# Optimization experiments

Measured on AMD Instinct MI355X. Metric: run time of the kernel, lower is better.

Reference implementation:

```python
import jax, jax.numpy as jnp
import numpy as np

V, C, L, NH, NKV, HID, E, K, T, B = 32000, 1536, 2, 12, 4, 2048, 8, 2, 2048, 1
D = C // NH  # 128
NREP = NH // NKV
EPS = 1e-6

def _rms(x, w):
    return x * jax.lax.rsqrt(jnp.mean(x * x, axis=-1, keepdims=True) + EPS) * w


def setup_inputs() -> dict:
    key = jax.random.key(0)
    ks = jax.random.split(key, 14)
    s = 0.02
    inp = {
        "tokens": jax.random.randint(ks[0], (B, T), 0, V, dtype=jnp.int64),
        "emb": jax.random.normal(ks[1], (V, C), jnp.float32) * s,      # tied with output proj
        "pos": jax.random.normal(ks[2], (T, C), jnp.float32) * s,
        "wq": jax.random.normal(ks[3], (L, C, NH * D), jnp.float32) * s,
        "wk": jax.random.normal(ks[4], (L, C, NKV * D), jnp.float32) * s,
        "wv": jax.random.normal(ks[5], (L, C, NKV * D), jnp.float32) * s,
        "wo": jax.random.normal(ks[6], (L, C, C), jnp.float32) * s,
        "attn_norm_w": jnp.ones((L, C), jnp.float32),
        "ffn_norm_w": jnp.ones((L, C), jnp.float32),
        "gate": jax.random.normal(ks[7], (L, C, E), jnp.float32) * s,
        "ew1": jax.random.normal(ks[8], (L, E, C, HID), jnp.float32) * s,
        "ew2": jax.random.normal(ks[9], (L, E, HID, C), jnp.float32) * s,
        "ew3": jax.random.normal(ks[10], (L, E, C, HID), jnp.float32) * s,
        "final_norm_w": jnp.ones((C,), jnp.float32),
    }
    return inp


def _forward(tokens, emb, pos, wq, wk, wv, wo, attn_norm_w, ffn_norm_w, gate,
             ew1, ew2, ew3, final_norm_w):
    x = emb[tokens] + pos[None, :T]            # [B,T,C]; dropout=0 (eval)
    causal = jnp.tril(jnp.ones((T, T), bool))
    for l in range(L):
        # --- GQA attention ---
        h = _rms(x, attn_norm_w[l])
        q = (h @ wq[l]).reshape(B, T, NH, D).transpose(0, 2, 1, 3)     # [B,NH,T,D]
        k = (h @ wk[l]).reshape(B, T, NKV, D).transpose(0, 2, 1, 3)
        v = (h @ wv[l]).reshape(B, T, NKV, D).transpose(0, 2, 1, 3)
        k = jnp.repeat(k, NREP, axis=1)
        v = jnp.repeat(v, NREP, axis=1)
        scores = jnp.einsum("bhqd,bhkd->bhqk", q, k) / jnp.sqrt(jnp.float32(D))
        scores = jnp.where(causal, scores, jnp.finfo(scores.dtype).min)
        attn = jax.nn.softmax(scores, axis=-1)
        y = jnp.einsum("bhqk,bhkd->bhqd", attn, v)
        y = y.transpose(0, 2, 1, 3).reshape(B, T, C)
        x = x + y @ wo[l]
        # --- MoE FFN (top-k routed SwiGLU experts) ---
        xf = _rms(x, ffn_norm_w[l]).reshape(-1, C)                      # [N,C]
        probs = jax.nn.softmax(xf @ gate[l], axis=-1)                   # [N,E]
        topw, topi = jax.lax.top_k(probs, K)
        topw = topw / jnp.sum(topw, axis=-1, keepdims=True)
        dense_w = jnp.sum(jax.nn.one_hot(topi, E, dtype=xf.dtype) * topw[..., None], axis=1)  # [N,E]
        h1 = jnp.einsum("nc,ech->enh", xf, ew1[l])
        h3 = jnp.einsum("nc,ech->enh", xf, ew3[l])
        hh = jax.nn.silu(h1) * h3                                       # [E,N,HID]
        moe = jnp.einsum("ne,enh,ehc->nc", dense_w, hh, ew2[l])
        x = x + moe.reshape(B, T, C)
    x = _rms(x, final_norm_w)
    logits = x @ emb.T                                                   # tied output proj
    return logits


def reference(tokens, emb, pos, wq, wk, wv, wo, attn_norm_w, ffn_norm_w, gate,
              ew1, ew2, ew3, final_norm_w):
    return _forward(tokens, emb, pos, wq, wk, wv, wo, attn_norm_w, ffn_norm_w,
                    gate, ew1, ew2, ew3, final_norm_w)
```

## Files before the change

kernel.cpp:

```cpp
#include <hip/hip_runtime.h>
#include <hip/hip_bf16.h>
#include <math.h>

#define Tn   2048
#define Cn   1536
#define Vn   32000
#define NHn  12
#define NKVn 4
#define Dn   128
#define HIDn 2048
#define En   8
#define Kn   2
#define Ln   2
#define NREPn 3
#define EPSn 1e-6f
#define CHT  16
#define NCHn 4

using bf16 = __hip_bfloat16;
using bf16x8 = __attribute__((ext_vector_type(8))) short;
using f32x4v = __attribute__((ext_vector_type(4))) float;

__device__ __forceinline__ void split3(float v, short& h, short& m, short& lo) {
  bf16 b0 = __float2bfloat16(v);
  float r1 = v - __bfloat162float(b0);
  bf16 b1 = __float2bfloat16(r1);
  float r2 = r1 - __bfloat162float(b1);
  bf16 b2 = __float2bfloat16(r2);
  h = *reinterpret_cast<short*>(&b0);
  m = *reinterpret_cast<short*>(&b1);
  lo = *reinterpret_cast<short*>(&b2);
}
__device__ __forceinline__ float b2f(short s) {
  bf16 b = *reinterpret_cast<bf16*>(&s);
  return __bfloat162float(b);
}
__device__ __forceinline__ void gl_lds16(const void* g, void* l) {
  __builtin_amdgcn_global_load_lds((const __attribute__((address_space(1))) void*)g,
                                   (__attribute__((address_space(3))) void*)l, 16, 0, 0);
}

__global__ void embed_k(const int* __restrict__ tok, const float* __restrict__ emb,
                        const float* __restrict__ pos, float* __restrict__ x) {
  int n = blockIdx.x;
  int t = threadIdx.x;
  int id = tok[n];
  const float* er = emb + (size_t)id * Cn;
  const float* pr = pos + (size_t)n * Cn;
  float* xr = x + (size_t)n * Cn;
  for (int c = t; c < Cn; c += 256) xr[c] = er[c] + pr[c];
}

__global__ void rmsnorm_k(const float* __restrict__ x, const float* __restrict__ w,
                          float* __restrict__ out) {
  int n = blockIdx.x, t = threadIdx.x;
  const float* xr = x + (size_t)n * Cn;
  float v[6];
  float ss = 0.f;
#pragma unroll
  for (int i = 0; i < 6; i++) { v[i] = xr[t + i * 256]; ss += v[i] * v[i]; }
  for (int off = 32; off > 0; off >>= 1) ss += __shfl_down(ss, off, 64);
  __shared__ float red[4];
  __shared__ float rtot;
  int wave = t >> 6, lane = t & 63;
  if (lane == 0) red[wave] = ss;
  __syncthreads();
  if (t == 0) rtot = rsqrtf((red[0] + red[1] + red[2] + red[3]) / (float)Cn + EPSn);
  __syncthreads();
  float r = rtot;
  float* orow = out + (size_t)n * Cn;
#pragma unroll
  for (int i = 0; i < 6; i++) { int c = t + i * 256; orow[c] = v[i] * r * w[c]; }
}

__global__ void f2b_k(const float* __restrict__ s, bf16* __restrict__ d, size_t n4) {
  size_t i = (size_t)blockIdx.x * 256 + threadIdx.x;
  size_t stride = (size_t)gridDim.x * 256;
  for (; i < n4; i += stride) {
    float4 v = ((const float4*)s)[i];
    d[i * 4 + 0] = __float2bfloat16(v.x);
    d[i * 4 + 1] = __float2bfloat16(v.y);
    d[i * 4 + 2] = __float2bfloat16(v.z);
    d[i * 4 + 3] = __float2bfloat16(v.w);
  }
}

__global__ void splita_k(const float* __restrict__ s, short* __restrict__ dh,
                         short* __restrict__ dm, short* __restrict__ dl, size_t n4) {
  size_t i = (size_t)blockIdx.x * 256 + threadIdx.x;
  size_t stride = (size_t)gridDim.x * 256;
  for (; i < n4; i += stride) {
    float4 v = ((const float4*)s)[i];
    float a[4] = {v.x, v.y, v.z, v.w};
#pragma unroll
    for (int u = 0; u < 4; u++) {
      short h, m, lo;
      split3(a[u], h, m, lo);
      dh[i * 4 + u] = h; dm[i * 4 + u] = m; dl[i * 4 + u] = lo;
    }
  }
}

__global__ void transp3_k(const float* __restrict__ src, short* __restrict__ dh,
                          short* __restrict__ dm, short* __restrict__ dl, int K, int N) {
  __shared__ __align__(16) float ls[32][33];
// ... 133 lines not shown
      int ro = (wc + j * 16 + rl) * 32 + ko;
      bf16x8 bh = *(const bf16x8*)(sBH + ro);
      bf16x8 bm_ = *(const bf16x8*)(sBM + ro);
      bf16x8 bl = *(const bf16x8*)(sBL + ro);
#pragma unroll
      for (int i = 0; i < 4; i++) {
        acc[i][j] = __builtin_amdgcn_mfma_f32_16x16x32_bf16(aL[i], bh, acc[i][j], 0, 0, 0);
        acc[i][j] = __builtin_amdgcn_mfma_f32_16x16x32_bf16(aH[i], bl, acc[i][j], 0, 0, 0);
        acc[i][j] = __builtin_amdgcn_mfma_f32_16x16x32_bf16(aM[i], bm_, acc[i][j], 0, 0, 0);
        acc[i][j] = __builtin_amdgcn_mfma_f32_16x16x32_bf16(aM[i], bh, acc[i][j], 0, 0, 0);
        acc[i][j] = __builtin_amdgcn_mfma_f32_16x16x32_bf16(aH[i], bm_, acc[i][j], 0, 0, 0);
        acc[i][j] = __builtin_amdgcn_mfma_f32_16x16x32_bf16(aH[i], bh, acc[i][j], 0, 0, 0);
      }
    }
    __syncthreads();
  }
#pragma unroll
  for (int i = 0; i < 4; i++) {
    int rbase = bm + wr + i * 16 + (l >> 4) * 4;
#pragma unroll
    for (int j = 0; j < 4; j++) {
      int col = bn + wc + j * 16 + (l & 15);
#pragma unroll
      for (int r = 0; r < 4; r++) {
        size_t idx = (size_t)(rbase + r) * N + col;
        float v = acc[i][j][r];
        if (res) v += res[idx];
        Co[idx] = v;
      }
    }
  }
}

__global__ void __launch_bounds__(256) mexp6(const bf16* __restrict__ AH, const bf16* __restrict__ AM,
                                             const bf16* __restrict__ AL,
                                             const bf16* __restrict__ BH, const bf16* __restrict__ BM,
                                             const bf16* __restrict__ BL,
                                             const int* __restrict__ perm, const int* __restrict__ cnt,
                                             int ebase,
                                             short* __restrict__ HH, short* __restrict__ HM,
                                             short* __restrict__ HL,
                                             float* __restrict__ Co, int K, int N, int mode) {
  int e = ebase + blockIdx.z;
  int nrows = cnt[e];
  int bm = blockIdx.x * 128;
  if (bm >= nrows) return;
  int bn = blockIdx.y * 128;
  size_t eoff = (size_t)blockIdx.z * K * N;
  __shared__ __align__(16) bf16 sAH[128 * 32], sAM[128 * 32], sAL[128 * 32];
  __shared__ __align__(16) bf16 sBH[128 * 32], sBM[128 * 32], sBL[128 * 32];
  __shared__ int prow[128];
  int t = threadIdx.x, l = t & 63, w = t >> 6;
  if (t < 128) {
    int i = bm + t;
    prow[t] = (i < nrows) ? perm[e * Tn + i] : -1;
  }
  __syncthreads();
  int wr = (w >> 1) * 64, wc = (w & 1) * 64;
  const f32x4v zero = {0.f, 0.f, 0.f, 0.f};
  f32x4v acc[4][4];
#pragma unroll
  for (int i = 0; i < 4; i++)
#pragma unroll
    for (int j = 0; j < 4; j++) acc[i][j] = zero;
  int p0 = prow[t >> 2], p1 = prow[64 + (t >> 2)];
  int g0r = (p0 >= 0) ? (mode == 2 ? p0 : (p0 >> 1)) : 0;
  int g1r = (p1 >= 0) ? (mode == 2 ? p1 : (p1 >> 1)) : 0;
  size_t a0 = (size_t)g0r * K + (t & 3) * 8;
  size_t a1 = (size_t)g1r * K + (t & 3) * 8;
  size_t b0 = eoff + (size_t)(bn + (t >> 2)) * K + (t & 3) * 8;
  size_t b1 = eoff + (size_t)(bn + 64 + (t >> 2)) * K + (t & 3) * 8;
  int rl = l & 15, ko = (l >> 4) * 8;
  for (int k0 = 0; k0 < K; k0 += 32) {
    gl_lds16(AH + a0 + k0, (char*)sAH + t * 16);
    gl_lds16(AH + a1 + k0, (char*)sAH + (256 + t) * 16);
    gl_lds16(AM + a0 + k0, (char*)sAM + t * 16);
    gl_lds16(AM + a1 + k0, (char*)sAM + (256 + t) * 16);
    gl_lds16(AL + a0 + k0, (char*)sAL + t * 16);
    gl_lds16(AL + a1 + k0, (char*)sAL + (256 + t) * 16);
    gl_lds16(BH + b0 + k0, (char*)sBH + t * 16);
    gl_lds16(BH + b1 + k0, (char*)sBH + (256 + t) * 16);
    gl_lds16(BM + b0 + k0, (char*)sBM + t * 16);
    gl_lds16(BM + b1 + k0, (char*)sBM + (256 + t) * 16);
    gl_lds16(BL + b0 + k0, (char*)sBL + t * 16);
    gl_lds16(BL + b1 + k0, (char*)sBL + (256 + t) * 16);
    __syncthreads();
    bf16x8 aH[4], aM[4], aL[4];
#pragma unroll
    for (int i = 0; i < 4; i++) {
      int ro = (wr + i * 16 + rl) * 32 + ko;
      aH[i] = *(const bf16x8*)(sAH + ro);
      aM[i] = *(const bf16x8*)(sAM + ro);
      aL[i] = *(const bf16x8*)(sAL + ro);
    }
#pragma unroll
    for (int j = 0; j < 4; j++) {
      int ro = (wc + j * 16 + rl) * 32 + ko;
      bf16x8 bh = *(const bf16x8*)(sBH + ro);
      bf16x8 bm_ = *(const bf16x8*)(sBM + ro);
      bf16x8 bl = *(const bf16x8*)(sBL + ro);
#pragma unroll
      for (int i = 0; i < 4; i++) {
        acc[i][j] = __builtin_amdgcn_mfma_f32_16x16x32_bf16(aL[i], bh, acc[i][j], 0, 0, 0);
        acc[i][j] = __builtin_amdgcn_mfma_f32_16x16x32_bf16(aH[i], bl, acc[i][j], 0, 0, 0);
        acc[i][j] = __builtin_amdgcn_mfma_f32_16x16x32_bf16(aM[i], bm_, acc[i][j], 0, 0, 0);
        acc[i][j] = __builtin_amdgcn_mfma_f32_16x16x32_bf16(aM[i], bh, acc[i][j], 0, 0, 0);
        acc[i][j] = __builtin_amdgcn_mfma_f32_16x16x32_bf16(aH[i], bm_, acc[i][j], 0, 0, 0);
        acc[i][j] = __builtin_amdgcn_mfma_f32_16x16x32_bf16(aH[i], bh, acc[i][j], 0, 0, 0);
      }
    }
    __syncthreads();
  }
#pragma unroll
  for (int i = 0; i < 4; i++) {
#pragma unroll
    for (int r = 0; r < 4; r++) {
      int lrow = wr + i * 16 + (l >> 4) * 4 + r;
      int p = prow[lrow];
      if (p < 0) continue;
#pragma unroll
      for (int j = 0; j < 4; j++) {
        int col = bn + wc + j * 16 + (l & 15);
        size_t idx = (size_t)p * N + col;
        float v = acc[i][j][r];
        if (mode == 0) {
          short h, m, lo;
          split3(v, h, m, lo);
          HH[idx] = h; HM[idx] = m; HL[idx] = lo;
        } else if (mode == 1) {
          float v1 = b2f(HH[idx]) + b2f(HM[idx]) + b2f(HL[idx]);
          float hh = (v1 / (1.f + expf(-v1))) * v;
          short h, m, lo;
          split3(hh, h, m, lo);
          HH[idx] = h; HM[idx] = m; HL[idx] = lo;
        } else {
          Co[idx] = v;
        }
      }
    }
  }
}

__global__ void __launch_bounds__(256) mexpB(const bf16* __restrict__ A, const bf16* __restrict__ B,
                                             const int* __restrict__ perm, const int* __restrict__ cnt,
                                             int ebase, bf16* __restrict__ HB,
                                             float* __restrict__ Co, int K, int N, int mode) {
  int e = ebase + blockIdx.z;
  int nrows = cnt[e];
  int bm = blockIdx.x * 128;
  if (bm >= nrows) return;
  int bn = blockIdx.y * 128;
  size_t eoff = (size_t)blockIdx.z * K * N;
  __shared__ __align__(16) bf16 sA[128 * 32];
  __shared__ __align__(16) bf16 sB[128 * 32];
  __shared__ int prow[128];
  int t = threadIdx.x, l = t & 63, w = t >> 6;
  if (t < 128) {
    int i = bm + t;
    prow[t] = (i < nrows) ? perm[e * Tn + i] : -1;
  }
  __syncthreads();
  int wr = (w >> 1) * 64, wc = (w & 1) * 64;
  const f32x4v zero = {0.f, 0.f, 0.f, 0.f};
  f32x4v acc[4][4];
#pragma unroll
  for (int i = 0; i < 4; i++)
#pragma unroll
    for (int j = 0; j < 4; j++) acc[i][j] = zero;
  int p0 = prow[t >> 2], p1 = prow[64 + (t >> 2)];
  int g0r = (p0 >= 0) ? (mode == 2 ? p0 : (p0 >> 1)) : 0;
  int g1r = (p1 >= 0) ? (mode == 2 ? p1 : (p1 >> 1)) : 0;
  size_t a0 = (size_t)g0r * K + (t & 3) * 8;
  size_t a1 = (size_t)g1r * K + (t & 3) * 8;
  size_t b0 = eoff + (size_t)(bn + (t >> 2)) * K + (t & 3) * 8;
  size_t b1 = eoff + (size_t)(bn + 64 + (t >> 2)) * K + (t & 3) * 8;
  int rl = l & 15, ko = (l >> 4) * 8;
  for (int k0 = 0; k0 < K; k0 += 32) {
    gl_lds16(A + a0 + k0, (char*)sA + t * 16);
    gl_lds16(A + a1 + k0, (char*)sA + (256 + t) * 16);
    gl_lds16(B + b0 + k0, (char*)sB + t * 16);
    gl_lds16(B + b1 + k0, (char*)sB + (256 + t) * 16);
    __syncthreads();
    bf16x8 a[4], b[4];
#pragma unroll
    for (int i = 0; i < 4; i++) a[i] = *(const bf16x8*)(sA + (wr + i * 16 + rl) * 32 + ko);
#pragma unroll
    for (int j = 0; j < 4; j++) b[j] = *(const bf16x8*)(sB + (wc + j * 16 + rl) * 32 + ko);
#pragma unroll
    for (int i = 0; i < 4; i++)
#pragma unroll
      for (int j = 0; j < 4; j++)
        acc[i][j] = __builtin_amdgcn_mfma_f32_16x16x32_bf16(a[i], b[j], acc[i][j], 0, 0, 0);
    __syncthreads();
  }
#pragma unroll
  for (int i = 0; i < 4; i++) {
#pragma unroll
    for (int r = 0; r < 4; r++) {
      int lrow = wr + i * 16 + (l >> 4) * 4 + r;
      int p = prow[lrow];
      if (p < 0) continue;
#pragma unroll
      for (int j = 0; j < 4; j++) {
        int col = bn + wc + j * 16 + (l & 15);
        size_t idx = (size_t)p * N + col;
        float v = acc[i][j][r];
        if (mode == 0) {
          HB[idx] = __float2bfloat16(v);
        } else if (mode == 1) {
          float v1 = __bfloat162float(HB[idx]);
          HB[idx] = __float2bfloat16((v1 / (1.f + expf(-v1))) * v);
        } else {
          Co[idx] = v;
        }
      }
    }
  }
}

__global__ void __launch_bounds__(256) attn_part_k(const float* __restrict__ q,
                                                   const float* __restrict__ k,
                                                   const float* __restrict__ v,
                                                   float* __restrict__ po,
                                                   float* __restrict__ pm,
                                                   float* __restrict__ pl) {
  int qt = blockIdx.x;
  int head = blockIdx.y;
  int ch = blockIdx.z;
  int ntiles = qt + 1;
  int tA = ch * CHT;
  if (tA >= ntiles) return;
  int tB = tA + CHT < ntiles ? tA + CHT : ntiles;
  int kvh = head / NREPn;
  int q0 = qt * 32;
  int t = threadIdx.x;
  int r = t >> 3, g = t & 7, d0 = g * 16;
  int row = q0 + r;
  __shared__ __align__(16) float ks[32][Dn + 4];
  __shared__ __align__(16) float vs[32][Dn + 4];
  const float scale = 0.08838834764831845f;
  float qr[16];
  {
    const float* qrow = q + (size_t)row * (NHn * Dn) + head * Dn + d0;
#pragma unroll
    for (int j = 0; j < 16; j += 4) {
      float4 u = *(const float4*)(qrow + j);
      qr[j] = u.x * scale; qr[j + 1] = u.y * scale;
      qr[j + 2] = u.z * scale; qr[j + 3] = u.w * scale;
    }
  }
  float o[16];
#pragma unroll
  for (int j = 0; j < 16; j++) o[j] = 0.f;
  float rowm = -1e30f, rowl = 0.f;

  for (int kt = tA; kt < tB; kt++) {
    int kv0 = kt * 32;
    for (int e = t; e < 32 * 32; e += 256) {
      int rr = e >> 5, c4 = (e & 31) * 4;
      size_t off = (size_t)(kv0 + rr) * (NKVn * Dn) + kvh * Dn + c4;
      *(float4*)&ks[rr][c4] = *(const float4*)(k + off);
      *(float4*)&vs[rr][c4] = *(const float4*)(v + off);
    }
    __syncthreads();
    float s[32];
#pragma unroll
    for (int kk = 0; kk < 32; kk++) {
      const float* krow = &ks[kk][d0];
      float p = 0.f;
#pragma unroll
      for (int j = 0; j < 16; j += 4) {
        float4 u = *(const float4*)(krow + j);
        p += qr[j] * u.x + qr[j + 1] * u.y + qr[j + 2] * u.z + qr[j + 3] * u.w;
      }
      p += __shfl_xor(p, 1);
      p += __shfl_xor(p, 2);
      p += __shfl_xor(p, 4);
      s[kk] = p;
    }
    if (kt == qt) {
#pragma unroll
      for (int kk = 0; kk < 32; kk++)
        if (kk > r) s[kk] = -1e30f;
    }
    float mx = s[0];
#pragma unroll
    for (int kk = 1; kk < 32; kk++) mx = fmaxf(mx, s[kk]);
    float m_new = fmaxf(rowm, mx);
    float corr = expf(rowm - m_new);
    float sum = 0.f;
#pragma unroll
    for (int kk = 0; kk < 32; kk++) { s[kk] = expf(s[kk] - m_new); sum += s[kk]; }
    rowl = rowl * corr + sum;
    rowm = m_new;
#pragma unroll
// ... 128 lines not shown
  const float* pos    = (const float*)d_in[2];
  const float* wq     = (const float*)d_in[3];
  const float* wk     = (const float*)d_in[4];
  const float* wv     = (const float*)d_in[5];
  const float* wo     = (const float*)d_in[6];
  const float* attn_nw= (const float*)d_in[7];
  const float* ffn_nw = (const float*)d_in[8];
  const float* gate   = (const float*)d_in[9];
  const float* ew1    = (const float*)d_in[10];
  const float* ew2    = (const float*)d_in[11];
  const float* ew3    = (const float*)d_in[12];
  const float* final_nw = (const float*)d_in[13];
  float* out = (float*)d_out;

  char* wsb = (char*)d_ws;
  const size_t NC = (size_t)Tn * Cn;
  size_t off = 0;
  auto alloc = [&](size_t bytes) -> size_t {
    off = (off + 255) & ~(size_t)255;
    size_t p = off;
    off += bytes;
    return p;
  };
  size_t o_x    = alloc(NC * 4);
  size_t o_h    = alloc(NC * 4);
  size_t o_gl   = alloc((size_t)Tn * En * 4);
  size_t o_topw = alloc((size_t)Tn * Kn * 4);
  size_t o_cnt  = alloc(64);
  size_t o_perm = alloc((size_t)En * Tn * 4);
  size_t wlvl   = (size_t)4 * Cn * HIDn * 2;
  size_t o_w    = alloc(3 * wlvl);
  size_t hs_lvl = NC * 2;
  size_t o_hs   = alloc(3 * hs_lvl);
  size_t o_qb   = alloc(NC * 4);
  size_t o_kb   = alloc((size_t)Tn * NKVn * Dn * 4);
  size_t o_vb   = alloc((size_t)Tn * NKVn * Dn * 4);
  size_t o_yb   = alloc(NC * 4);
  size_t hb_lvl = (size_t)Tn * Kn * HIDn * 2;
  size_t o_hbs  = o_qb;
  size_t end_hbs = o_hbs + 3 * hb_lvl;
  if (off < end_hbs) off = end_hbs;
  size_t o_pair = alloc(NC * 4);
  size_t o_po   = alloc((size_t)NHn * Tn * NCHn * Dn * 4);
  size_t o_pm   = alloc((size_t)NHn * Tn * NCHn * 4);
  size_t o_pl   = alloc((size_t)NHn * Tn * NCHn * 4);

  float* x       = (float*)(wsb + o_x);
  float* h       = (float*)(wsb + o_h);
  float* gl      = (float*)(wsb + o_gl);
  float* topw    = (float*)(wsb + o_topw);
  int*   cnt     = (int*)(wsb + o_cnt);
  int*   perm    = (int*)(wsb + o_perm);
  float* qb      = (float*)(wsb + o_qb);
  float* kb      = (float*)(wsb + o_kb);
  float* vb      = (float*)(wsb + o_vb);
  float* yb      = (float*)(wsb + o_yb);
  float* pairout = (float*)(wsb + o_pair);
  bf16*  hb      = (bf16*)(wsb + o_pair);
  bf16*  embB    = (bf16*)(wsb + o_w);
  float* po      = (float*)(wsb + o_po);
  float* pm      = (float*)(wsb + o_pm);
  float* pl      = (float*)(wsb + o_pl);

  short* hs[3]; short* hbs[3]; short* ewT[3];
  for (int s = 0; s < 3; s++) {
    hs[s]  = (short*)(wsb + o_hs + (size_t)s * hs_lvl);
    hbs[s] = (short*)(wsb + o_hbs + (size_t)s * hb_lvl);
    ewT[s] = (short*)(wsb + o_w + (size_t)s * wlvl);
  }
  size_t wq_lvl = (size_t)Cn * (NHn * Dn) * 2;
  size_t wk_lvl = (size_t)Cn * (NKVn * Dn) * 2;
  short* wqT[3]; short* wkT[3]; short* wvT[3]; short* woT[3];
  {
    size_t p = o_w;
    for (int s = 0; s < 3; s++) { wqT[s] = (short*)(wsb + p); p += wq_lvl; }
    for (int s = 0; s < 3; s++) { wkT[s] = (short*)(wsb + p); p += wk_lvl; }
    for (int s = 0; s < 3; s++) { wvT[s] = (short*)(wsb + p); p += wk_lvl; }
    for (int s = 0; s < 3; s++) { woT[s] = (short*)(wsb + p); p += wq_lvl; }
  }

  embed_k<<<Tn, 256, 0, stream>>>(tokens, emb, pos, x);
  for (int l = 0; l < Ln; l++) {
    const float* wq_l = wq + (size_t)l * Cn * (NHn * Dn);
    const float* wk_l = wk + (size_t)l * Cn * (NKVn * Dn);
    const float* wv_l = wv + (size_t)l * Cn * (NKVn * Dn);
    const float* wo_l = wo + (size_t)l * Cn * Cn;
    const float* g_l  = gate + (size_t)l * Cn * En;
    const float* e1_l = ew1 + (size_t)l * En * Cn * HIDn;
    const float* e2_l = ew2 + (size_t)l * En * HIDn * Cn;
    const float* e3_l = ew3 + (size_t)l * En * Cn * HIDn;

    transp3_k<<<dim3(Cn / 32, (NHn * Dn) / 32, 1), 256, 0, stream>>>(wq_l, wqT[0], wqT[1], wqT[2], Cn, NHn * Dn);
    transp3_k<<<dim3(Cn / 32, (NKVn * Dn) / 32, 1), 256, 0, stream>>>(wk_l, wkT[0], wkT[1], wkT[2], Cn, NKVn * Dn);
    transp3_k<<<dim3(Cn / 32, (NKVn * Dn) / 32, 1), 256, 0, stream>>>(wv_l, wvT[0], wvT[1], wvT[2], Cn, NKVn * Dn);
    transp3_k<<<dim3(Cn / 32, Cn / 32, 1), 256, 0, stream>>>(wo_l, woT[0], woT[1], woT[2], Cn, Cn);
    rmsnorm_k<<<Tn, 256, 0, stream>>>(x, attn_nw + (size_t)l * Cn, h);
    splita_k<<<2048, 256, 0, stream>>>(h, hs[0], hs[1], hs[2], NC / 4);
    gemm6<<<dim3(Tn / 128, (NHn * Dn) / 128), 256, 0, stream>>>(
        (bf16*)hs[0], (bf16*)hs[1], (bf16*)hs[2], (bf16*)wqT[0], (bf16*)wqT[1], (bf16*)wqT[2],
        nullptr, qb, Tn, NHn * Dn, Cn);
    gemm6<<<dim3(Tn / 128, (NKVn * Dn) / 128), 256, 0, stream>>>(
        (bf16*)hs[0], (bf16*)hs[1], (bf16*)hs[2], (bf16*)wkT[0], (bf16*)wkT[1], (bf16*)wkT[2],
        nullptr, kb, Tn, NKVn * Dn, Cn);
    gemm6<<<dim3(Tn / 128, (NKVn * Dn) / 128), 256, 0, stream>>>(
        (bf16*)hs[0], (bf16*)hs[1], (bf16*)hs[2], (bf16*)wvT[0], (bf16*)wvT[1], (bf16*)wvT[2],
        nullptr, vb, Tn, NKVn * Dn, Cn);
    attn_part_k<<<dim3(Tn / 32, NHn, NCHn), 256, 0, stream>>>(qb, kb, vb, po, pm, pl);
    attn_merge_k<<<dim3(Tn / 32, NHn), 256, 0, stream>>>(po, pm, pl, yb);
    splita_k<<<2048, 256, 0, stream>>>(yb, hs[0], hs[1], hs[2], NC / 4);
    gemm6<<<dim3(Tn / 128, Cn / 128), 256, 0, stream>>>(
        (bf16*)hs[0], (bf16*)hs[1], (bf16*)hs[2], (bf16*)woT[0], (bf16*)woT[1], (bf16*)woT[2],
        x, x, Tn, Cn, Cn);

    rmsnorm_k<<<Tn, 256, 0, stream>>>(x, ffn_nw + (size_t)l * Cn, h);
    gate_k<<<Tn, 256, 0, stream>>>(h, g_l, gl);
    hipMemsetAsync(cnt, 0, 64, stream);
    route_k<<<Tn / 256, 256, 0, stream>>>(gl, topw, cnt, perm);

    if (l < Ln - 1) {
      splita_k<<<2048, 256, 0, stream>>>(h, hs[0], hs[1], hs[2], NC / 4);
      for (int half = 0; half < 2; half++) {
        size_t hoff = (size_t)half * 4 * Cn * HIDn;
        int eb = half * 4;
        transp3_k<<<dim3(Cn / 32, HIDn / 32, 4), 256, 0, stream>>>(e1_l + hoff, ewT[0], ewT[1], ewT[2], Cn, HIDn);
        mexp6<<<dim3(Tn / 128, HIDn / 128, 4), 256, 0, stream>>>(
            (bf16*)hs[0], (bf16*)hs[1], (bf16*)hs[2], (bf16*)ewT[0], (bf16*)ewT[1], (bf16*)ewT[2],
            perm, cnt, eb, hbs[0], hbs[1], hbs[2], nullptr, Cn, HIDn, 0);
        transp3_k<<<dim3(Cn / 32, HIDn / 32, 4), 256, 0, stream>>>(e3_l + hoff, ewT[0], ewT[1], ewT[2], Cn, HIDn);
        mexp6<<<dim3(Tn / 128, HIDn / 128, 4), 256, 0, stream>>>(
            (bf16*)hs[0], (bf16*)hs[1], (bf16*)hs[2], (bf16*)ewT[0], (bf16*)ewT[1], (bf16*)ewT[2],
            perm, cnt, eb, hbs[0], hbs[1], hbs[2], nullptr, Cn, HIDn, 1);
        transp3_k<<<dim3(HIDn / 32, Cn / 32, 4), 256, 0, stream>>>(e2_l + hoff, ewT[0], ewT[1], ewT[2], HIDn, Cn);
        mexp6<<<dim3(Tn / 128, Cn / 128, 4), 256, 0, stream>>>(
            (bf16*)hbs[0], (bf16*)hbs[1], (bf16*)hbs[2], (bf16*)ewT[0], (bf16*)ewT[1], (bf16*)ewT[2],
            perm, cnt, eb, hbs[0], hbs[1], hbs[2], pairout, HIDn, Cn, 2);
      }
    } else {
      f2b_k<<<2048, 256, 0, stream>>>(h, (bf16*)hs[0], NC / 4);
      for (int half = 0; half < 2; half++) {
        size_t hoff = (size_t)half * 4 * Cn * HIDn;
        int eb = half * 4;
        transp_k<<<dim3(Cn / 32, HIDn / 32, 4), 256, 0, stream>>>(e1_l + hoff, (bf16*)ewT[0], Cn, HIDn);
        mexpB<<<dim3(Tn / 128, HIDn / 128, 4), 256, 0, stream>>>(
            (bf16*)hs[0], (bf16*)ewT[0], perm, cnt, eb, (bf16*)hbs[0], nullptr, Cn, HIDn, 0);
        transp_k<<<dim3(Cn / 32, HIDn / 32, 4), 256, 0, stream>>>(e3_l + hoff, (bf16*)ewT[0], Cn, HIDn);
        mexpB<<<dim3(Tn / 128, HIDn / 128, 4), 256, 0, stream>>>(
            (bf16*)hs[0], (bf16*)ewT[0], perm, cnt, eb, (bf16*)hbs[0], nullptr, Cn, HIDn, 1);
        transp_k<<<dim3(HIDn / 32, Cn / 32, 4), 256, 0, stream>>>(e2_l + hoff, (bf16*)ewT[0], HIDn, Cn);
        mexpB<<<dim3(Tn / 128, Cn / 128, 4), 256, 0, stream>>>(
            (bf16*)hbs[0], (bf16*)ewT[0], perm, cnt, eb, (bf16*)hbs[0], pairout, HIDn, Cn, 2);
      }
    }
    combine_k<<<Tn, 256, 0, stream>>>(pairout, topw, x);
  }
  rmsnorm_k<<<Tn, 256, 0, stream>>>(x, final_nw, h);
  f2b_k<<<2048, 256, 0, stream>>>(h, hb, NC / 4);
  f2b_k<<<2048, 256, 0, stream>>>(emb, embB, (size_t)Vn * Cn / 4);
  gemm_btl<<<dim3(Tn / 128, Vn / 128), 256, 0, stream>>>(hb, embB, nullptr, out, Tn, Vn, Cn);
}
```

Baseline: 5.301 ms.

## Fuse QKV projections, dual gate/up expert GEMMs, and rmsnorm with split conversion

Concatenates the Q, K and V weights into one transposed matrix so a single GEMM writes a packed QKV buffer, which attention reads at fixed offsets. The expert w1 and w3 GEMMs are merged into one kernel that keeps two accumulators and applies SiLU-multiply in its epilogue, so the activation is no longer written, read back and re-split. RMSNorm now emits the bf16 or three-way bf16 split directly, removing separate splita and f2b passes. The cost is higher register and LDS use in the dual kernels, which may lower occupancy, and the split-precision expert path is now processed two experts at a time.

```diff
diff --git a/kernel.cpp b/kernel.cpp
--- a/kernel.cpp
+++ b/kernel.cpp
@@ -16,6 +16,7 @@
 #define EPSn 1e-6f
 #define CHT  16
 #define NCHn 4
+#define QKVW 2560
 
 using bf16 = __hip_bfloat16;
 using bf16x8 = __attribute__((ext_vector_type(8))) short;
@@ -51,8 +52,9 @@
   for (int c = t; c < Cn; c += 256) xr[c] = er[c] + pr[c];
 }
 
-__global__ void rmsnorm_k(const float* __restrict__ x, const float* __restrict__ w,
-                          float* __restrict__ out) {
+__global__ void rms3_k(const float* __restrict__ x, const float* __restrict__ w,
+                       float* __restrict__ outf, short* __restrict__ dh,
+                       short* __restrict__ dm, short* __restrict__ dl) {
   int n = blockIdx.x, t = threadIdx.x;
   const float* xr = x + (size_t)n * Cn;
   float v[6];
@@ -68,9 +70,43 @@
   if (t == 0) rtot = rsqrtf((red[0] + red[1] + red[2] + red[3]) / (float)Cn + EPSn);
   __syncthreads();
   float r = rtot;
-  float* orow = out + (size_t)n * Cn;
-#pragma unroll
-  for (int i = 0; i < 6; i++) { int c = t + i * 256; orow[c] = v[i] * r * w[c]; }
+#pragma unroll
+  for (int i = 0; i < 6; i++) {
+    int c = t + i * 256;
+    float val = v[i] * r * w[c];
+    size_t idx = (size_t)n * Cn + c;
+    if (outf) outf[idx] = val;
+    short h, m, lo;
+    split3(val, h, m, lo);
+    dh[idx] = h; dm[idx] = m; dl[idx] = lo;
+  }
+}
+
+__global__ void rmsb_k(const float* __restrict__ x, const float* __restrict__ w,
+                       float* __restrict__ outf, bf16* __restrict__ outb) {
+  int n = blockIdx.x, t = threadIdx.x;
+  const float* xr = x + (size_t)n * Cn;
+  float v[6];
+  float ss = 0.f;
+#pragma unroll
+  for (int i = 0; i < 6; i++) { v[i] = xr[t + i * 256]; ss += v[i] * v[i]; }
+  for (int off = 32; off > 0; off >>= 1) ss += __shfl_down(ss, off, 64);
+  __shared__ float red[4];
+  __shared__ float rtot;
+  int wave = t >> 6, lane = t & 63;
+  if (lane == 0) red[wave] = ss;
+  __syncthreads();
+  if (t == 0) rtot = rsqrtf((red[0] + red[1] + red[2] + red[3]) / (float)Cn + EPSn);
+  __syncthreads();
+  float r = rtot;
+#pragma unroll
+  for (int i = 0; i < 6; i++) {
+    int c = t + i * 256;
+    float val = v[i] * r * w[c];
+    size_t idx = (size_t)n * Cn + c;
+    if (outf) outf[idx] = val;
+    outb[idx] = __float2bfloat16(val);
+  }
 }
 
 __global__ void f2b_k(const float* __restrict__ s, bf16* __restrict__ d, size_t n4) {
@@ -270,15 +306,132 @@
   }
 }
 
+__global__ void __launch_bounds__(256) mexp6d(const bf16* __restrict__ AH, const bf16* __restrict__ AM,
+                                              const bf16* __restrict__ AL,
+                                              const bf16* __restrict__ B1H, const bf16* __restrict__ B1M,
+                                              const bf16* __restrict__ B1L,
+                                              const bf16* __restrict__ B3H, const bf16* __restrict__ B3M,
+                                              const bf16* __restrict__ B3L,
+                                              const int* __restrict__ perm, const int* __restrict__ cnt,
+                                              int ebase,
+                                              short* __restrict__ HH, short* __restrict__ HM,
+                                              short* __restrict__ HL, int K, int N) {
+  int e = ebase + blockIdx.z;
+  int nrows = cnt[e];
+  int bm = blockIdx.x * 128;
+  if (bm >= nrows) return;
+  int bn = blockIdx.y * 128;
+  size_t eoff = (size_t)blockIdx.z * K * N;
+  __shared__ __align__(16) bf16 sAH[128 * 32], sAM[128 * 32], sAL[128 * 32];
+  __shared__ __align__(16) bf16 s1H[128 * 32], s1M[128 * 32], s1L[128 * 32];
+  __shared__ __align__(16) bf16 s3H[128 * 32], s3M[128 * 32], s3L[128 * 32];
+  __shared__ int prow[128];
+  int t = threadIdx.x, l = t & 63, w = t >> 6;
+  if (t < 128) {
+    int i = bm + t;
+    prow[t] = (i < nrows) ? perm[e * Tn + i] : -1;
+  }
+  __syncthreads();
+  int wr = (w >> 1) * 64, wc = (w & 1) * 64;
+  const f32x4v zero = {0.f, 0.f, 0.f, 0.f};
+  f32x4v acc1[4][4], acc3[4][4];
+#pragma unroll
+  for (int i = 0; i < 4; i++)
+#pragma unroll
+    for (int j = 0; j < 4; j++) { acc1[i][j] = zero; acc3[i][j] = zero; }
+  int p0 = prow[t >> 2], p1 = prow[64 + (t >> 2)];
+  int g0r = (p0 >= 0) ? (p0 >> 1) : 0;
+  int g1r = (p1 >= 0) ? (p1 >> 1) : 0;
+  size_t a0 = (size_t)g0r * K + (t & 3) * 8;
+  size_t a1 = (size_t)g1r * K + (t & 3) * 8;
+  size_t b0 = eoff + (size_t)(bn + (t >> 2)) * K + (t & 3) * 8;
+  size_t b1 = eoff + (size_t)(bn + 64 + (t >> 2)) * K + (t & 3) * 8;
+  int rl = l & 15, ko = (l >> 4) * 8;
+  for (int k0 = 0; k0 < K; k0 += 32) {
+    gl_lds16(AH + a0 + k0, (char*)sAH + t * 16);
+    gl_lds16(AH + a1 + k0, (char*)sAH + (256 + t) * 16);
+    gl_lds16(AM + a0 + k0, (char*)sAM + t * 16);
+    gl_lds16(AM + a1 + k0, (char*)sAM + (256 + t) * 16);
+    gl_lds16(AL + a0 + k0, (char*)sAL + t * 16);
+    gl_lds16(AL + a1 + k0, (char*)sAL + (256 + t) * 16);
+    gl_lds16(B1H + b0 + k0, (char*)s1H + t * 16);
+    gl_lds16(B1H + b1 + k0, (char*)s1H + (256 + t) * 16);
+    gl_lds16(B1M + b0 + k0, (char*)s1M + t * 16);
+    gl_lds16(B1M + b1 + k0, (char*)s1M + (256 + t) * 16);
+    gl_lds16(B1L + b0 + k0, (char*)s1L + t * 16);
+    gl_lds16(B1L + b1 + k0, (char*)s1L + (256 + t) * 16);
+    gl_lds16(B3H + b0 + k0, (char*)s3H + t * 16);
+    gl_lds16(B3H + b1 + k0, (char*)s3H + (256 + t) * 16);
+    gl_lds16(B3M + b0 + k0, (char*)s3M + t * 16);
+    gl_lds16(B3M + b1 + k0, (char*)s3M + (256 + t) * 16);
+    gl_lds16(B3L + b0 + k0, (char*)s3L + t * 16);
+    gl_lds16(B3L + b1 + k0, (char*)s3L + (256 + t) * 16);
+    __syncthreads();
+    bf16x8 aH[4], aM[4], aL[4];
+#pragma unroll
+    for (int i = 0; i < 4; i++) {
+      int ro = (wr + i * 16 + rl) * 32 + ko;
+      aH[i] = *(const bf16x8*)(sAH + ro);
+      aM[i] = *(const bf16x8*)(sAM + ro);
+      aL[i] = *(const bf16x8*)(sAL + ro);
+    }
+#pragma unroll
+    for (int j = 0; j < 4; j++) {
+      int ro = (wc + j * 16 + rl) * 32 + ko;
+      bf16x8 bh = *(const bf16x8*)(s1H + ro);
+      bf16x8 bm_ = *(const bf16x8*)(s1M + ro);
+      bf16x8 bl = *(const bf16x8*)(s1L + ro);
+#pragma unroll
+      for (int i = 0; i < 4; i++) {
+        acc1[i][j] = __builtin_amdgcn_mfma_f32_16x16x32_bf16(aL[i], bh, acc1[i][j], 0, 0, 0);
+        acc1[i][j] = __builtin_amdgcn_mfma_f32_16x16x32_bf16(aH[i], bl, acc1[i][j], 0, 0, 0);
+        acc1[i][j] = __builtin_amdgcn_mfma_f32_16x16x32_bf16(aM[i], bm_, acc1[i][j], 0, 0, 0);
+        acc1[i][j] = __builtin_amdgcn_mfma_f32_16x16x32_bf16(aM[i], bh, acc1[i][j], 0, 0, 0);
+        acc1[i][j] = __builtin_amdgcn_mfma_f32_16x16x32_bf16(aH[i], bm_, acc1[i][j], 0, 0, 0);
+        acc1[i][j] = __builtin_amdgcn_mfma_f32_16x16x32_bf16(aH[i], bh, acc1[i][j], 0, 0, 0);
+      }
+      bh = *(const bf16x8*)(s3H + ro);
+      bm_ = *(const bf16x8*)(s3M + ro);
+      bl = *(const bf16x8*)(s3L + ro);
+#pragma unroll
+      for (int i = 0; i < 4; i++) {
+        acc3[i][j] = __builtin_amdgcn_mfma_f32_16x16x32_bf16(aL[i], bh, acc3[i][j], 0, 0, 0);
+        acc3[i][j] = __builtin_amdgcn_mfma_f32_16x16x32_bf16(aH[i], bl, acc3[i][j], 0, 0, 0);
+        acc3[i][j] = __builtin_amdgcn_mfma_f32_16x16x32_bf16(aM[i], bm_, acc3[i][j], 0, 0, 0);
+        acc3[i][j] = __builtin_amdgcn_mfma_f32_16x16x32_bf16(aM[i], bh, acc3[i][j], 0, 0, 0);
+        acc3[i][j] = __builtin_amdgcn_mfma_f32_16x16x32_bf16(aH[i], bm_, acc3[i][j], 0, 0, 0);
+        acc3[i][j] = __builtin_amdgcn_mfma_f32_16x16x32_bf16(aH[i], bh, acc3[i][j], 0, 0, 0);
+      }
+    }
+    __syncthreads();
+  }
+#pragma unroll
+  for (int i = 0; i < 4; i++) {
+#pragma unroll
+    for (int r = 0; r < 4; r++) {
+      int lrow = wr + i * 16 + (l >> 4) * 4 + r;
+      int p = prow[lrow];
+      if (p < 0) continue;
+#pragma unroll
+      for (int j = 0; j < 4; j++) {
+        int col = bn + wc + j * 16 + (l & 15);
+        size_t idx = (size_t)p * N + col;
+        float h1 = acc1[i][j][r], h3 = acc3[i][j][r];
+        float hh = (h1 / (1.f + expf(-h1))) * h3;
+        short h, m, lo;
+        split3(hh, h, m, lo);
+        HH[idx] = h; HM[idx] = m; HL[idx] = lo;
+      }
+    }
+  }
+}
+
 __global__ void __launch_bounds__(256) mexp6(const bf16* __restrict__ AH, const bf16* __restrict__ AM,
                                              const bf16* __restrict__ AL,
                                              const bf16* __restrict__ BH, const bf16* __restrict__ BM,
                                              const bf16* __restrict__ BL,
                                              const int* __restrict__ perm, const int* __restrict__ cnt,
-                                             int ebase,
-                                             short* __restrict__ HH, short* __restrict__ HM,
-                                             short* __restrict__ HL,
-                                             float* __restrict__ Co, int K, int N, int mode) {
+                                             int ebase, float* __restrict__ Co, int K, int N) {
   int e = ebase + blockIdx.z;
   int nrows = cnt[e];
   int bm = blockIdx.x * 128;
@@ -302,8 +455,8 @@
 #pragma unroll
     for (int j = 0; j < 4; j++) acc[i][j] = zero;
   int p0 = prow[t >> 2], p1 = prow[64 + (t >> 2)];
-  int g0r = (p0 >= 0) ? (mode == 2 ? p0 : (p0 >> 1)) : 0;
-  int g1r = (p1 >= 0) ? (mode == 2 ? p1 : (p1 >> 1)) : 0;
+  int g0r = (p0 >= 0) ? p0 : 0;
+  int g1r = (p1 >= 0) ? p1 : 0;
   size_t a0 = (size_t)g0r * K + (t & 3) * 8;
   size_t a1 = (size_t)g1r * K + (t & 3) * 8;
   size_t b0 = eoff + (size_t)(bn + (t >> 2)) * K + (t & 3) * 8;
@@ -359,21 +512,83 @@
 #pragma unroll
       for (int j = 0; j < 4; j++) {
         int col = bn + wc + j * 16 + (l & 15);
-        size_t idx = (size_t)p * N + col;
-        float v = acc[i][j][r];
-        if (mode == 0) {
-          short h, m, lo;
-          split3(v, h, m, lo);
-          HH[idx] = h; HM[idx] = m; HL[idx] = lo;
-        } else if (mode == 1) {
-          float v1 = b2f(HH[idx]) + b2f(HM[idx]) + b2f(HL[idx]);
-          float hh = (v1 / (1.f + expf(-v1))) * v;
-          short h, m, lo;
-          split3(hh, h, m, lo);
-          HH[idx] = h; HM[idx] = m; HL[idx] = lo;
-        } else {
-          Co[idx] = v;
-        }
+        Co[(size_t)p * N + col] = acc[i][j][r];
+      }
+    }
+  }
+}
+
+__global__ void __launch_bounds__(256) mexpBd(const bf16* __restrict__ A, const bf16* __restrict__ B1,
+                                              const bf16* __restrict__ B3,
+                                              const int* __restrict__ perm, const int* __restrict__ cnt,
+                                              int ebase, bf16* __restrict__ HB, int K, int N) {
+  int e = ebase + blockIdx.z;
+  int nrows = cnt[e];
+  int bm = blockIdx.x * 128;
+  if (bm >= nrows) return;
+  int bn = blockIdx.y * 128;
+  size_t eoff = (size_t)blockIdx.z * K * N;
+  __shared__ __align__(16) bf16 sA[128 * 32];
+  __shared__ __align__(16) bf16 s1[128 * 32];
+  __shared__ __align__(16) bf16 s3[128 * 32];
+  __shared__ int prow[128];
+  int t = threadIdx.x, l = t & 63, w = t >> 6;
+  if (t < 128) {
+    int i = bm + t;
+    prow[t] = (i < nrows) ? perm[e * Tn + i] : -1;
+  }
+  __syncthreads();
+  int wr = (w >> 1) * 64, wc = (w & 1) * 64;
+  const f32x4v zero = {0.f, 0.f, 0.f, 0.f};
+  f32x4v acc1[4][4], acc3[4][4];
+#pragma unroll
+  for (int i = 0; i < 4; i++)
+#pragma unroll
+    for (int j = 0; j < 4; j++) { acc1[i][j] = zero; acc3[i][j] = zero; }
+  int p0 = prow[t >> 2], p1 = prow[64 + (t >> 2)];
+  int g0r = (p0 >= 0) ? (p0 >> 1) : 0;
+  int g1r = (p1 >= 0) ? (p1 >> 1) : 0;
+  size_t a0 = (size_t)g0r * K + (t & 3) * 8;
+  size_t a1 = (size_t)g1r * K + (t & 3) * 8;
+  size_t b0 = eoff + (size_t)(bn + (t >> 2)) * K + (t & 3) * 8;
+  size_t b1 = eoff + (size_t)(bn + 64 + (t >> 2)) * K + (t & 3) * 8;
+  int rl = l & 15, ko = (l >> 4) * 8;
+  for (int k0 = 0; k0 < K; k0 += 32) {
+    gl_lds16(A + a0 + k0, (char*)sA + t * 16);
+    gl_lds16(A + a1 + k0, (char*)sA + (256 + t) * 16);
+    gl_lds16(B1 + b0 + k0, (char*)s1 + t * 16);
+    gl_lds16(B1 + b1 + k0, (char*)s1 + (256 + t) * 16);
+    gl_lds16(B3 + b0 + k0, (char*)s3 + t * 16);
+    gl_lds16(B3 + b1 + k0, (char*)s3 + (256 + t) * 16);
+    __syncthreads();
+    bf16x8 a[4];
+#pragma unroll
+    for (int i = 0; i < 4; i++) a[i] = *(const bf16x8*)(sA + (wr + i * 16 + rl) * 32 + ko);
+#pragma unroll
+    for (int j = 0; j < 4; j++) {
+      int ro = (wc + j * 16 + rl) * 32 + ko;
+      bf16x8 b1v = *(const bf16x8*)(s1 + ro);
+      bf16x8 b3v = *(const bf16x8*)(s3 + ro);
+#pragma unroll
+      for (int i = 0; i < 4; i++) {
+        acc1[i][j] = __builtin_amdgcn_mfma_f32_16x16x32_bf16(a[i], b1v, acc1[i][j], 0, 0, 0);
+        acc3[i][j] = __builtin_amdgcn_mfma_f32_16x16x32_bf16(a[i], b3v, acc3[i][j], 0, 0, 0);
+      }
+    }
+    __syncthreads();
+  }
+#pragma unroll
+  for (int i = 0; i < 4; i++) {
+#pragma unroll
+    for (int r = 0; r < 4; r++) {
+      int lrow = wr + i * 16 + (l >> 4) * 4 + r;
+      int p = prow[lrow];
+      if (p < 0) continue;
+#pragma unroll
+      for (int j = 0; j < 4; j++) {
+        int col = bn + wc + j * 16 + (l & 15);
+        float h1 = acc1[i][j][r], h3 = acc3[i][j][r];
+        HB[(size_t)p * N + col] = __float2bfloat16((h1 / (1.f + expf(-h1))) * h3);
       }
     }
   }
@@ -381,8 +596,7 @@
 
 __global__ void __launch_bounds__(256) mexpB(const bf16* __restrict__ A, const bf16* __restrict__ B,
                                              const int* __restrict__ perm, const int* __restrict__ cnt,
-                                             int ebase, bf16* __restrict__ HB,
-                                             float* __restrict__ Co, int K, int N, int mode) {
+                                             int ebase, float* __restrict__ Co, int K, int N) {
   int e = ebase + blockIdx.z;
   int nrows = cnt[e];
   int bm = blockIdx.x * 128;
@@ -406,8 +620,8 @@
 #pragma unroll
     for (int j = 0; j < 4; j++) acc[i][j] = zero;
   int p0 = prow[t >> 2], p1 = prow[64 + (t >> 2)];
-  int g0r = (p0 >= 0) ? (mode == 2 ? p0 : (p0 >> 1)) : 0;
-  int g1r = (p1 >= 0) ? (mode == 2 ? p1 : (p1 >> 1)) : 0;
+  int g0r = (p0 >= 0) ? p0 : 0;
+  int g1r = (p1 >= 0) ? p1 : 0;
   size_t a0 = (size_t)g0r * K + (t & 3) * 8;
   size_t a1 = (size_t)g1r * K + (t & 3) * 8;
   size_t b0 = eoff + (size_t)(bn + (t >> 2)) * K + (t & 3) * 8;
@@ -441,24 +655,13 @@
 #pragma unroll
       for (int j = 0; j < 4; j++) {
         int col = bn + wc + j * 16 + (l & 15);
-        size_t idx = (size_t)p * N + col;
-        float v = acc[i][j][r];
-        if (mode == 0) {
-          HB[idx] = __float2bfloat16(v);
-        } else if (mode == 1) {
-          float v1 = __bfloat162float(HB[idx]);
-          HB[idx] = __float2bfloat16((v1 / (1.f + expf(-v1))) * v);
-        } else {
-          Co[idx] = v;
-        }
-      }
-    }
-  }
-}
-
-__global__ void __launch_bounds__(256) attn_part_k(const float* __restrict__ q,
-                                                   const float* __restrict__ k,
-                                                   const float* __restrict__ v,
+        Co[(size_t)p * N + col] = acc[i][j][r];
+      }
+    }
+  }
+}
+
+__global__ void __launch_bounds__(256) attn_part_k(const float* __restrict__ qkv,
                                                    float* __restrict__ po,
                                                    float* __restrict__ pm,
                                                    float* __restrict__ pl) {
@@ -479,7 +682,7 @@
   const float scale = 0.08838834764831845f;
   float qr[16];
   {
-    const float* qrow = q + (size_t)row * (NHn * Dn) + head * Dn + d0;
+    const float* qrow = qkv + (size_t)row * QKVW + head * Dn + d0;
 #pragma unroll
     for (int j = 0; j < 16; j += 4) {
       float4 u = *(const float4*)(qrow + j);
@@ -496,9 +699,9 @@
     int kv0 = kt * 32;
     for (int e = t; e < 32 * 32; e += 256) {
       int rr = e >> 5, c4 = (e & 31) * 4;
-      size_t off = (size_t)(kv0 + rr) * (NKVn * Dn) + kvh * Dn + c4;
-      *(float4*)&ks[rr][c4] = *(const float4*)(k + off);
-      *(float4*)&vs[rr][c4] = *(const float4*)(v + off);
+      size_t base = (size_t)(kv0 + rr) * QKVW + kvh * Dn + c4;
+      *(float4*)&ks[rr][c4] = *(const float4*)(qkv + base + 1536);
+      *(float4*)&vs[rr][c4] = *(const float4*)(qkv + base + 2048);
     }
     __syncthreads();
     float s[32];
@@ -693,12 +896,10 @@
   size_t o_w    = alloc(3 * wlvl);
   size_t hs_lvl = NC * 2;
   size_t o_hs   = alloc(3 * hs_lvl);
-  size_t o_qb   = alloc(NC * 4);
-  size_t o_kb   = alloc((size_t)Tn * NKVn * Dn * 4);
-  size_t o_vb   = alloc((size_t)Tn * NKVn * Dn * 4);
+  size_t o_qkv  = alloc((size_t)Tn * QKVW * 4);
   size_t o_yb   = alloc(NC * 4);
   size_t hb_lvl = (size_t)Tn * Kn * HIDn * 2;
-  size_t o_hbs  = o_qb;
+  size_t o_hbs  = o_qkv;
   size_t end_hbs = o_hbs + 3 * hb_lvl;
   if (off < end_hbs) off = end_hbs;
   size_t o_pair = alloc(NC * 4);
@@ -712,9 +913,7 @@
   float* topw    = (float*)(wsb + o_topw);
   int*   cnt     = (int*)(wsb + o_cnt);
   int*   perm    = (int*)(wsb + o_perm);
-  float* qb      = (float*)(wsb + o_qb);
-  float* kb      = (float*)(wsb + o_kb);
-  float* vb      = (float*)(wsb + o_vb);
+  float* qkvb    = (float*)(wsb + o_qkv);
   float* yb      = (float*)(wsb + o_yb);
   float* pairout = (float*)(wsb + o_pair);
   bf16*  hb      = (bf16*)(wsb + o_pair);
@@ -723,22 +922,28 @@
   float* pm      = (float*)(wsb + o_pm);
   float* pl      = (float*)(wsb + o_pl);
 
-  short* hs[3]; short* hbs[3]; short* ewT[3];
+  short* hs[3]; short* hbs[3];
   for (int s = 0; s < 3; s++) {
     hs[s]  = (short*)(wsb + o_hs + (size_t)s * hs_lvl);
     hbs[s] = (short*)(wsb + o_hbs + (size_t)s * hb_lvl);
-    ewT[s] = (short*)(wsb + o_w + (size_t)s * wlvl);
-  }
-  size_t wq_lvl = (size_t)Cn * (NHn * Dn) * 2;
-  size_t wk_lvl = (size_t)Cn * (NKVn * Dn) * 2;
-  short* wqT[3]; short* wkT[3]; short* wvT[3]; short* woT[3];
-  {
-    size_t p = o_w;
-    for (int s = 0; s < 3; s++) { wqT[s] = (short*)(wsb + p); p += wq_lvl; }
-    for (int s = 0; s < 3; s++) { wkT[s] = (short*)(wsb + p); p += wk_lvl; }
-    for (int s = 0; s < 3; s++) { wvT[s] = (short*)(wsb + p); p += wk_lvl; }
-    for (int s = 0; s < 3; s++) { woT[s] = (short*)(wsb + p); p += wq_lvl; }
-  }
+  }
+  size_t qkvw_lvl = (size_t)QKVW * Cn * 2;
+  size_t wo_lvl   = (size_t)Cn * Cn * 2;
+  short* qkvT[3]; short* woT[3];
+  for (int s = 0; s < 3; s++) {
+    qkvT[s] = (short*)(wsb + o_w + (size_t)s * qkvw_lvl);
+    woT[s]  = (short*)(wsb + o_w + 3 * qkvw_lvl + (size_t)s * wo_lvl);
+  }
+  size_t q2lvl = (size_t)2 * Cn * HIDn * 2;
+  short* e1T[3]; short* e3T[3]; short* e2T[3];
+  for (int s = 0; s < 3; s++) {
+    e1T[s] = (short*)(wsb + o_w + (size_t)s * q2lvl);
+    e3T[s] = (short*)(wsb + o_w + 3 * q2lvl + (size_t)s * q2lvl);
+    e2T[s] = (short*)(wsb + o_w + (size_t)s * wlvl);
+  }
+  bf16* ew1B = (bf16*)(wsb + o_w);
+  bf16* ew3B = (bf16*)(wsb + o_w + wlvl);
+  bf16* ew2B = (bf16*)(wsb + o_w);
 
   embed_k<<<Tn, 256, 0, stream>>>(tokens, emb, pos, x);
   for (int l = 0; l < Ln; l++) {
@@ -751,71 +956,67 @@
     const float* e2_l = ew2 + (size_t)l * En * HIDn * Cn;
     const float* e3_l = ew3 + (size_t)l * En * Cn * HIDn;
 
-    transp3_k<<<dim3(Cn / 32, (NHn * Dn) / 32, 1), 256, 0, stream>>>(wq_l, wqT[0], wqT[1], wqT[2], Cn, NHn * Dn);
-    transp3_k<<<dim3(Cn / 32, (NKVn * Dn) / 32, 1), 256, 0, stream>>>(wk_l, wkT[0], wkT[1], wkT[2], Cn, NKVn * Dn);
-    transp3_k<<<dim3(Cn / 32, (NKVn * Dn) / 32, 1), 256, 0, stream>>>(wv_l, wvT[0], wvT[1], wvT[2], Cn, NKVn * Dn);
+    transp3_k<<<dim3(Cn / 32, (NHn * Dn) / 32, 1), 256, 0, stream>>>(wq_l, qkvT[0], qkvT[1], qkvT[2], Cn, NHn * Dn);
+    transp3_k<<<dim3(Cn / 32, (NKVn * Dn) / 32, 1), 256, 0, stream>>>(
+        wk_l, qkvT[0] + (size_t)1536 * Cn, qkvT[1] + (size_t)1536 * Cn, qkvT[2] + (size_t)1536 * Cn, Cn, NKVn * Dn);
+    transp3_k<<<dim3(Cn / 32, (NKVn * Dn) / 32, 1), 256, 0, stream>>>(
+        wv_l, qkvT[0] + (size_t)2048 * Cn, qkvT[1] + (size_t)2048 * Cn, qkvT[2] + (size_t)2048 * Cn, Cn, NKVn * Dn);
     transp3_k<<<dim3(Cn / 32, Cn / 32, 1), 256, 0, stream>>>(wo_l, woT[0], woT[1], woT[2], Cn, Cn);
-    rmsnorm_k<<<Tn, 256, 0, stream>>>(x, attn_nw + (size_t)l * Cn, h);
-    splita_k<<<2048, 256, 0, stream>>>(h, hs[0], hs[1], hs[2], NC / 4);
-    gemm6<<<dim3(Tn / 128, (NHn * Dn) / 128), 256, 0, stream>>>(
-        (bf16*)hs[0], (bf16*)hs[1], (bf16*)hs[2], (bf16*)wqT[0], (bf16*)wqT[1], (bf16*)wqT[2],
-        nullptr, qb, Tn, NHn * Dn, Cn);
-    gemm6<<<dim3(Tn / 128, (NKVn * Dn) / 128), 256, 0, stream>>>(
-        (bf16*)hs[0], (bf16*)hs[1], (bf16*)hs[2], (bf16*)wkT[0], (bf16*)wkT[1], (bf16*)wkT[2],
-        nullptr, kb, Tn, NKVn * Dn, Cn);
-    gemm6<<<dim3(Tn / 128, (NKVn * Dn) / 128), 256, 0, stream>>>(
-        (bf16*)hs[0], (bf16*)hs[1], (bf16*)hs[2], (bf16*)wvT[0], (bf16*)wvT[1], (bf16*)wvT[2],
-        nullptr, vb, Tn, NKVn * Dn, Cn);
-    attn_part_k<<<dim3(Tn / 32, NHn, NCHn), 256, 0, stream>>>(qb, kb, vb, po, pm, pl);
+    rms3_k<<<Tn, 256, 0, stream>>>(x, attn_nw + (size_t)l * Cn, nullptr, hs[0], hs[1], hs[2]);
+    gemm6<<<dim3(Tn / 128, QKVW / 128), 256, 0, stream>>>(
+        (bf16*)hs[0], (bf16*)hs[1], (bf16*)hs[2], (bf16*)qkvT[0], (bf16*)qkvT[1], (bf16*)qkvT[2],
+        nullptr, qkvb, Tn, QKVW, Cn);
+    attn_part_k<<<dim3(Tn / 32, NHn, NCHn), 256, 0, stream>>>(qkvb, po, pm, pl);
     attn_merge_k<<<dim3(Tn / 32, NHn), 256, 0, stream>>>(po, pm, pl, yb);
     splita_k<<<2048, 256, 0, stream>>>(yb, hs[0], hs[1], hs[2], NC / 4);
     gemm6<<<dim3(Tn / 128, Cn / 128), 256, 0, stream>>>(
         (bf16*)hs[0], (bf16*)hs[1], (bf16*)hs[2], (bf16*)woT[0], (bf16*)woT[1], (bf16*)woT[2],
         x, x, Tn, Cn, Cn);
 
-    rmsnorm_k<<<Tn, 256, 0, stream>>>(x, ffn_nw + (size_t)l * Cn, h);
-    gate_k<<<Tn, 256, 0, stream>>>(h, g_l, gl);
-    hipMemsetAsync(cnt, 0, 64, stream);
-    route_k<<<Tn / 256, 256, 0, stream>>>(gl, topw, cnt, perm);
-
     if (l < Ln - 1) {
-      splita_k<<<2048, 256, 0, stream>>>(h, hs[0], hs[1], hs[2], NC / 4);
+      rms3_k<<<Tn, 256, 0, stream>>>(x, ffn_nw + (size_t)l * Cn, h, hs[0], hs[1], hs[2]);
+      gate_k<<<Tn, 256, 0, stream>>>(h, g_l, gl);
+      hipMemsetAsync(cnt, 0, 64, stream);
+      route_k<<<Tn / 256, 256, 0, stream>>>(gl, topw, cnt, perm);
+      for (int q = 0; q < 4; q++) {
+        size_t qoff = (size_t)q * 2 * Cn * HIDn;
+        transp3_k<<<dim3(Cn / 32, HIDn / 32, 2), 256, 0, stream>>>(e1_l + qoff, e1T[0], e1T[1], e1T[2], Cn, HIDn);
+        transp3_k<<<dim3(Cn / 32, HIDn / 32, 2), 256, 0, stream>>>(e3_l + qoff, e3T[0], e3T[1], e3T[2], Cn, HIDn);
+        mexp6d<<<dim3(Tn / 128, HIDn / 128, 2), 256, 0, stream>>>(
+            (bf16*)hs[0], (bf16*)hs[1], (bf16*)hs[2],
+            (bf16*)e1T[0], (bf16*)e1T[1], (bf16*)e1T[2],
+            (bf16*)e3T[0], (bf16*)e3T[1], (bf16*)e3T[2],
+            perm, cnt, q * 2, hbs[0], hbs[1], hbs[2], Cn, HIDn);
+      }
+      for (int half = 0; half < 2; half++) {
+        size_t hoff = (size_t)half * 4 * HIDn * Cn;
+        transp3_k<<<dim3(HIDn / 32, Cn / 32, 4), 256, 0, stream>>>(e2_l + hoff, e2T[0], e2T[1], e2T[2], HIDn, Cn);
+        mexp6<<<dim3(Tn / 128, Cn / 128, 4), 256, 0, stream>>>(
+            (bf16*)hbs[0], (bf16*)hbs[1], (bf16*)hbs[2], (bf16*)e2T[0], (bf16*)e2T[1], (bf16*)e2T[2],
+            perm, cnt, half * 4, pairout, HIDn, Cn);
+      }
+    } else {
+      bf16* hbf = (bf16*)hs[0];
+      bf16* hbB = (bf16*)hbs[0];
+      rmsb_k<<<Tn, 256, 0, stream>>>(x, ffn_nw + (size_t)l * Cn, h, hbf);
+      gate_k<<<Tn, 256, 0, stream>>>(h, g_l, gl);
+      hipMemsetAsync(cnt, 0, 64, stream);
+      route_k<<<Tn / 256, 256, 0, stream>>>(gl, topw, cnt, perm);
       for (int half = 0; half < 2; half++) {
         size_t hoff = (size_t)half * 4 * Cn * HIDn;
         int eb = half * 4;
-        transp3_k<<<dim3(Cn / 32, HIDn / 32, 4), 256, 0, stream>>>(e1_l + hoff, ewT[0], ewT[1], ewT[2], Cn, HIDn);
-        mexp6<<<dim3(Tn / 128, HIDn / 128, 4), 256, 0, stream>>>(
-            (bf16*)hs[0], (bf16*)hs[1], (bf16*)hs[2], (bf16*)ewT[0], (bf16*)ewT[1], (bf16*)ewT[2],
-            perm, cnt, eb, hbs[0], hbs[1], hbs[2], nullptr, Cn, HIDn, 0);
-        transp3_k<<<dim3(Cn / 32, HIDn / 32, 4), 256, 0, stream>>>(e3_l + hoff, ewT[0], ewT[1], ewT[2], Cn, HIDn);
-        mexp6<<<dim3(Tn / 128, HIDn / 128, 4), 256, 0, stream>>>(
-            (bf16*)hs[0], (bf16*)hs[1], (bf16*)hs[2], (bf16*)ewT[0], (bf16*)ewT[1], (bf16*)ewT[2],
-            perm, cnt, eb, hbs[0], hbs[1], hbs[2], nullptr, Cn, HIDn, 1);
-        transp3_k<<<dim3(HIDn / 32, Cn / 32, 4), 256, 0, stream>>>(e2_l + hoff, ewT[0], ewT[1], ewT[2], HIDn, Cn);
-        mexp6<<<dim3(Tn / 128, Cn / 128, 4), 256, 0, stream>>>(
-            (bf16*)hbs[0], (bf16*)hbs[1], (bf16*)hbs[2], (bf16*)ewT[0], (bf16*)ewT[1], (bf16*)ewT[2],
-            perm, cnt, eb, hbs[0], hbs[1], hbs[2], pairout, HIDn, Cn, 2);
-      }
-    } else {
-      f2b_k<<<2048, 256, 0, stream>>>(h, (bf16*)hs[0], NC / 4);
-      for (int half = 0; half < 2; half++) {
-        size_t hoff = (size_t)half * 4 * Cn * HIDn;
-        int eb = half * 4;
-        transp_k<<<dim3(Cn / 32, HIDn / 32, 4), 256, 0, stream>>>(e1_l + hoff, (bf16*)ewT[0], Cn, HIDn);
-        mexpB<<<dim3(Tn / 128, HIDn / 128, 4), 256, 0, stream>>>(
-            (bf16*)hs[0], (bf16*)ewT[0], perm, cnt, eb, (bf16*)hbs[0], nullptr, Cn, HIDn, 0);
-        transp_k<<<dim3(Cn / 32, HIDn / 32, 4), 256, 0, stream>>>(e3_l + hoff, (bf16*)ewT[0], Cn, HIDn);
-        mexpB<<<dim3(Tn / 128, HIDn / 128, 4), 256, 0, stream>>>(
-            (bf16*)hs[0], (bf16*)ewT[0], perm, cnt, eb, (bf16*)hbs[0], nullptr, Cn, HIDn, 1);
-        transp_k<<<dim3(HIDn / 32, Cn / 32, 4), 256, 0, stream>>>(e2_l + hoff, (bf16*)ewT[0], HIDn, Cn);
+        transp_k<<<dim3(Cn / 32, HIDn / 32, 4), 256, 0, stream>>>(e1_l + hoff, ew1B, Cn, HIDn);
+        transp_k<<<dim3(Cn / 32, HIDn / 32, 4), 256, 0, stream>>>(e3_l + hoff, ew3B, Cn, HIDn);
+        mexpBd<<<dim3(Tn / 128, HIDn / 128, 4), 256, 0, stream>>>(
+            hbf, ew1B, ew3B, perm, cnt, eb, hbB, Cn, HIDn);
+        transp_k<<<dim3(HIDn / 32, Cn / 32, 4), 256, 0, stream>>>(e2_l + (size_t)half * 4 * HIDn * Cn, ew2B, HIDn, Cn);
         mexpB<<<dim3(Tn / 128, Cn / 128, 4), 256, 0, stream>>>(
-            (bf16*)hbs[0], (bf16*)ewT[0], perm, cnt, eb, (bf16*)hbs[0], pairout, HIDn, Cn, 2);
+            hbB, ew2B, perm, cnt, eb, pairout, HIDn, Cn);
       }
     }
     combine_k<<<Tn, 256, 0, stream>>>(pairout, topw, x);
   }
-  rmsnorm_k<<<Tn, 256, 0, stream>>>(x, final_nw, h);
-  f2b_k<<<2048, 256, 0, stream>>>(h, hb, NC / 4);
+  rmsb_k<<<Tn, 256, 0, stream>>>(x, final_nw, nullptr, hb);
   f2b_k<<<2048, 256, 0, stream>>>(emb, embB, (size_t)Vn * Cn / 4);
   gemm_btl<<<dim3(Tn / 128, Vn / 128), 256, 0, stream>>>(hb, embB, nullptr, out, Tn, Vn, Cn);
 }
```

After: 5.360 ms. Within noise of the previous version (+1.1%).
